# Optimization experiments

Measured on AMD Instinct MI355X. Metric: run time of the kernel, lower is better.

## Reference

```python
import jax, jax.numpy as jnp
import numpy as np

N, GS, M = 128, 4, 64
C_IN, D, L = 128, 512, 8
LIN_D, OUT_DIM = 128, 1


def _gml_layer(G, h, W, b):
    # h: [N,M,C], W: [GS,P,C], b: [GS,P], G: [N,GS,M,M]
    multi = jnp.einsum('nmc,gpc->gnmp', h, W) + b[:, None, None, :]  # [GS,N,M,P]
    xo = jnp.einsum('ngij,gnjp->ngip', G, multi)                      # [N,GS,M,P]
    xo = jax.nn.relu(xo)
    return jnp.max(xo, axis=1)                                        # goodmax over GS


def setup_inputs() -> dict:
    key = jax.random.key(0)
    ks = jax.random.split(key, 12)
    s = 0.05
    return {
        'G': jax.random.uniform(ks[0], (N, GS, M, M), dtype=jnp.float32),
        'x': jax.random.normal(ks[1], (N, M, C_IN), dtype=jnp.float32),
        'W0': jax.random.normal(ks[2], (GS, D, C_IN), dtype=jnp.float32) * s,
        'b0': jax.random.normal(ks[3], (GS, D), dtype=jnp.float32) * s,
        'W': jax.random.normal(ks[4], (L - 1, GS, D, D), dtype=jnp.float32) * s,
        'b': jax.random.normal(ks[5], (L - 1, GS, D), dtype=jnp.float32) * s,
        'lin1_w': jax.random.normal(ks[6], (LIN_D, D), dtype=jnp.float32) * s,
        'lin1_b': jax.random.normal(ks[7], (LIN_D,), dtype=jnp.float32) * s,
        'lin2_w': jax.random.normal(ks[8], (OUT_DIM, LIN_D), dtype=jnp.float32) * s,
        'lin2_b': jax.random.normal(ks[9], (OUT_DIM,), dtype=jnp.float32) * s,
    }


def reference(G, x, W0, b0, W, b, lin1_w, lin1_b, lin2_w, lin2_b):
    # layer 0: C_IN -> D, shapes differ so no residual
    h = _gml_layer(G, x, W0, b0)  # [N,M,D]

    def step(h, wb):
        w, bb = wb
        return _gml_layer(G, h, w, bb) + h, None  # resnet residual (same shape)

    h, _ = jax.lax.scan(step, h, (W, b))  # L-1 layers of D -> D

    x1 = jnp.einsum('nmd,ed->nme', h, lin1_w) + lin1_b
    x2 = jnp.einsum('nme,oe->nmo', jax.nn.relu(x1), lin2_w) + lin2_b
    return x2  # [N, M, OUT_DIM]
```

## Files before the change

kernel.cpp:

```cpp
#include <hip/hip_runtime.h>

typedef float f32x4 __attribute__((ext_vector_type(4)));
typedef short s16x8 __attribute__((ext_vector_type(8)));
typedef short s16x4 __attribute__((ext_vector_type(4)));
typedef int   i32x4 __attribute__((ext_vector_type(4)));

using abfrag = s16x8;

#define DI __device__ __forceinline__

DI unsigned short f2bf(float x) {
  unsigned u = __builtin_bit_cast(unsigned, x);
  u += 0x7fffu + ((u >> 16) & 1u);
  return (unsigned short)(u >> 16);
}
DI float bf2f(unsigned short h) {
  return __builtin_bit_cast(float, ((unsigned)h) << 16);
}

DI f32x4 MFMA(abfrag a, abfrag b, f32x4 c) {
  return __builtin_amdgcn_mfma_f32_16x16x32_bf16(a, b, c, 0, 0, 0);
}

DI void gld16(void* lds_base, const void* gsrc) {
  __builtin_amdgcn_global_load_lds(
      (const __attribute__((address_space(1))) unsigned int*)gsrc,
      (__attribute__((address_space(3))) unsigned int*)lds_base, 16, 0, 0);
}

__global__ void f2bf_multi(const float* __restrict__ s0, int n0,
                           const float* __restrict__ s1, int n1,
                           const float* __restrict__ s2, int n2,
                           const float* __restrict__ s3, int n3,
                           unsigned short* __restrict__ dst) {
  const int total = n0 + n1 + n2 + n3;
  int i = blockIdx.x * blockDim.x + threadIdx.x;
  const int stride = gridDim.x * blockDim.x;
  for (; i < total; i += stride) {
    const float* s; int off;
    if (i < n0) { s = s0; off = i; }
    else if (i < n0 + n1) { s = s1; off = i - n0; }
    else if (i < n0 + n1 + n2) { s = s2; off = i - n0 - n1; }
    else { s = s3; off = i - n0 - n1 - n2; }
    f32x4 v = ((const f32x4*)s)[off];
    s16x4 o;
#pragma unroll
    for (int j = 0; j < 4; ++j) o[j] = (short)f2bf(v[j]);
    ((s16x4*)dst)[i] = o;
  }
}

template <int C, bool RES>
__global__ __launch_bounds__(256, 4) void gml_layer_kernel(
    const unsigned short* __restrict__ hin,
    const unsigned short* __restrict__ Wb,
    const float* __restrict__ bias,
    const unsigned short* __restrict__ Gb,
    unsigned short* __restrict__ hout) {
  constexpr int NT = C / 64;
  __shared__ short lh[64][64];
  __shared__ short lw[4][64][64];

  const int tid  = threadIdx.x;
  const int w    = tid >> 6;
  const int lane = tid & 63;
  const int l15  = lane & 15;
  const int l7   = l15 & 7;
  const int gq   = (lane >> 4) & 3;
  const int n    = blockIdx.x & 127;
  const int pc0  = (blockIdx.x >> 7) * 64;
  const int lrow = lane >> 3;
  const int s8   = lane & 7;
  const int lsoff = ((s8 ^ lrow) << 3);

  const unsigned short* hsrc = hin + (size_t)n * 64 * C;

  f32x4 acc[4][4];
#pragma unroll
  for (int g = 0; g < 4; ++g)
#pragma unroll
    for (int t = 0; t < 4; ++t) acc[g][t] = f32x4{0.f, 0.f, 0.f, 0.f};

  for (int kt = 0; kt < NT; ++kt) {
#pragma unroll
    for (int j = 0; j < 2; ++j)
      gld16(&lh[16 * w + 8 * j][0],
            hsrc + (size_t)(16 * w + 8 * j + lrow) * C + kt * 64 + lsoff);
#pragma unroll
    for (int j = 0; j < 8; ++j)
      gld16(&lw[w][8 * j][0],
            Wb + (size_t)(w * 512 + pc0 + 8 * j + lrow) * C + kt * 64 + lsoff);
    asm volatile("s_waitcnt vmcnt(0)" ::: "memory");
    __syncthreads();

#pragma unroll
    for (int ks = 0; ks < 2; ++ks) {
      const int so = ((4 * ks + gq) ^ l7) << 3;
      abfrag a[4];
#pragma unroll
      for (int t = 0; t < 4; ++t)
        a[t] = *(const abfrag*)&lh[16 * t + l15][so];
#pragma unroll
      for (int g = 0; g < 4; ++g) {
        const abfrag b = *(const abfrag*)&lw[g][16 * w + l15][so];
#pragma unroll
        for (int t = 0; t < 4; ++t) acc[g][t] = MFMA(a[t], b, acc[g][t]);
      }
    }
    __syncthreads();
  }

#pragma unroll
  for (int j = 0; j < 8; ++j)
    gld16(&lw[w][8 * j][0],
          Gb + (size_t)(n * 4 + w) * 4096 + (8 * j + lrow) * 64 + lsoff);
  asm volatile("s_waitcnt vmcnt(0)" ::: "memory");
  __syncthreads();

  float bv[4];
#pragma unroll
  for (int g = 0; g < 4; ++g) bv[g] = bias[g * 512 + pc0 + 16 * w + l15];

  f32x4 xmax[4];
#pragma unroll
  for (int t = 0; t < 4; ++t) xmax[t] = f32x4{0.f, 0.f, 0.f, 0.f};

#pragma unroll
  for (int g = 0; g < 4; ++g) {
    abfrag bb[2];
#pragma unroll
    for (int s = 0; s < 2; ++s) {
      abfrag t8;
#pragma unroll
      for (int r = 0; r < 4; ++r) {
        t8[r]     = (short)f2bf(acc[g][s][r] + bv[g]);
        t8[4 + r] = (short)f2bf(acc[g][s + 2][r] + bv[g]);
      }
      bb[s] = t8;
    }
#pragma unroll
    for (int t = 0; t < 4; ++t) {
      const short* grow = &lw[g][16 * t + l15][0];
      f32x4 xg = f32x4{0.f, 0.f, 0.f, 0.f};
#pragma unroll
      for (int s = 0; s < 2; ++s) {
        const int slot = 2 * s + (gq >> 1);
        const int e1 = ((slot ^ l7) << 3) + ((gq & 1) << 2);
        const int e2 = (((slot + 4) ^ l7) << 3) + ((gq & 1) << 2);
        s16x4 alo = *(const s16x4*)(grow + e1);
        s16x4 ahi = *(const s16x4*)(grow + e2);
        abfrag a;
#pragma unroll
        for (int j = 0; j < 4; ++j) { a[j] = alo[j]; a[4 + j] = ahi[j]; }
        xg = MFMA(a, bb[s], xg);
      }
#pragma unroll
      for (int r = 0; r < 4; ++r)
        xmax[t][r] = fmaxf(xmax[t][r], xg[r]);
    }
  }

  const int d = pc0 + 16 * w + l15;
#pragma unroll
  for (int t = 0; t < 4; ++t)
#pragma unroll
    for (int r = 0; r < 4; ++r) {
      const int m = 16 * t + 4 * gq + r;
      float v = xmax[t][r];
      if constexpr (RES) v += bf2f(hin[(size_t)(n * 64 + m) * C + d]);
      hout[(size_t)(n * 64 + m) * 512 + d] = f2bf(v);
    }
}

__global__ __launch_bounds__(256, 2) void final_kernel(
    const unsigned short* __restrict__ hin,
    const float* __restrict__ w1,
    const float* __restrict__ b1,
    const float* __restrict__ w2,
    const float* __restrict__ b2,
    float* __restrict__ out) {
  constexpr int KT = 64, LW = 72, C = 512, NT = C / KT;
  __shared__ short sh_h[2][64][LW];
  __shared__ short sh_w[2][128][LW];
  __shared__ float red[4][64];
  const int tid = threadIdx.x;
  const int wv  = tid >> 6;
  const int l15 = tid & 15;
  const int gq  = (tid >> 4) & 3;
  const int n   = blockIdx.x;
  const int srow = tid >> 3;
  const int scol = (tid & 7) * 8;
  const unsigned short* hsrc = hin + (size_t)n * 64 * C;

  f32x4 acc[4][2];
#pragma unroll
  for (int t = 0; t < 4; ++t)
#pragma unroll
    for (int u = 0; u < 2; ++u) acc[t][u] = f32x4{0.f, 0.f, 0.f, 0.f};

  i32x4 hr[2], wr[4];
#pragma unroll
  for (int p = 0; p < 2; ++p)
    hr[p] = *(const i32x4*)(hsrc + (srow + p * 32) * C + scol);
#pragma unroll
  for (int p = 0; p < 4; ++p) {
    const float* s = w1 + (srow + p * 32) * C + scol;
    f32x4 v0 = *(const f32x4*)s;
    f32x4 v1 = *(const f32x4*)(s + 4);
    s16x8 o;
#pragma unroll
    for (int j = 0; j < 4; ++j) { o[j] = (short)f2bf(v0[j]); o[4 + j] = (short)f2bf(v1[j]); }
    wr[p] = __builtin_bit_cast(i32x4, o);
  }
#pragma unroll
  for (int p = 0; p < 2; ++p) *(i32x4*)&sh_h[0][srow + p * 32][scol] = hr[p];
#pragma unroll
  for (int p = 0; p < 4; ++p) *(i32x4*)&sh_w[0][srow + p * 32][scol] = wr[p];

  for (int kt = 0; kt < NT; ++kt) {
    const int cur = kt & 1;
    if (kt + 1 < NT) {
#pragma unroll
      for (int p = 0; p < 2; ++p)
        hr[p] = *(const i32x4*)(hsrc + (srow + p * 32) * C + (kt + 1) * KT + scol);
#pragma unroll
      for (int p = 0; p < 4; ++p) {
        const float* s = w1 + (srow + p * 32) * C + (kt + 1) * KT + scol;
        f32x4 v0 = *(const f32x4*)s;
        f32x4 v1 = *(const f32x4*)(s + 4);
        s16x8 o;
#pragma unroll
        for (int j = 0; j < 4; ++j) { o[j] = (short)f2bf(v0[j]); o[4 + j] = (short)f2bf(v1[j]); }
        wr[p] = __builtin_bit_cast(i32x4, o);
      }
    }
    __syncthreads();
#pragma unroll
    for (int ks = 0; ks < 2; ++ks) {
      abfrag a[4], b[2];
#pragma unroll
      for (int t = 0; t < 4; ++t)
        a[t] = *(const abfrag*)&sh_h[cur][16 * t + l15][ks * 32 + gq * 8];
#pragma unroll
      for (int u = 0; u < 2; ++u)
        b[u] = *(const abfrag*)&sh_w[cur][32 * wv + 16 * u + l15][ks * 32 + gq * 8];
#pragma unroll
      for (int t = 0; t < 4; ++t)
#pragma unroll
        for (int u = 0; u < 2; ++u) acc[t][u] = MFMA(a[t], b[u], acc[t][u]);
    }
    if (kt + 1 < NT) {
#pragma unroll
      for (int p = 0; p < 2; ++p) *(i32x4*)&sh_h[1 - cur][srow + p * 32][scol] = hr[p];
#pragma unroll
      for (int p = 0; p < 4; ++p) *(i32x4*)&sh_w[1 - cur][srow + p * 32][scol] = wr[p];
    }
  }

  float b1v[2], w2v[2];
#pragma unroll
  for (int u = 0; u < 2; ++u) {
    b1v[u] = b1[32 * wv + 16 * u + l15];
    w2v[u] = w2[32 * wv + 16 * u + l15];
  }
  float part[4][4];
#pragma unroll
  for (int t = 0; t < 4; ++t)
#pragma unroll
    for (int r = 0; r < 4; ++r) {
      float s0 = 0.f;
#pragma unroll
      for (int u = 0; u < 2; ++u)
        s0 += fmaxf(acc[t][u][r] + b1v[u], 0.f) * w2v[u];
      part[t][r] = s0;
    }
#pragma unroll
  for (int t = 0; t < 4; ++t)
#pragma unroll
    for (int r = 0; r < 4; ++r)
#pragma unroll
      for (int msk = 1; msk < 16; msk <<= 1)
        part[t][r] += __shfl_xor(part[t][r], msk);
  if (l15 == 0) {
#pragma unroll
    for (int t = 0; t < 4; ++t)
#pragma unroll
      for (int r = 0; r < 4; ++r) red[wv][16 * t + 4 * gq + r] = part[t][r];
  }
  __syncthreads();
  if (tid < 64)
    out[(size_t)n * 64 + tid] =
        red[0][tid] + red[1][tid] + red[2][tid] + red[3][tid] + b2[0];
}

extern "C" void kernel_launch(void* const* d_in, const int* in_sizes, int n_in,
                              void* d_out, int out_size, void* d_ws, size_t ws_size,
                              hipStream_t stream) {
  const float* G   = (const float*)d_in[0];
  const float* x   = (const float*)d_in[1];
  const float* W0  = (const float*)d_in[2];
  const float* b0  = (const float*)d_in[3];
  const float* W   = (const float*)d_in[4];
  const float* b   = (const float*)d_in[5];
  const float* l1w = (const float*)d_in[6];
  const float* l1b = (const float*)d_in[7];
  const float* l2w = (const float*)d_in[8];
  const float* l2b = (const float*)d_in[9];
  float* out = (float*)d_out;

  char* p = (char*)d_ws;
  unsigned short* W0b = (unsigned short*)p; p += (size_t)4 * 512 * 128 * 2;
  unsigned short* Wb  = (unsigned short*)p; p += (size_t)7 * 4 * 512 * 512 * 2;
  unsigned short* Gb  = (unsigned short*)p; p += (size_t)128 * 4 * 64 * 64 * 2;
  unsigned short* xb  = (unsigned short*)p; p += (size_t)128 * 64 * 128 * 2;
  unsigned short* hA  = (unsigned short*)p; p += (size_t)128 * 64 * 512 * 2;
  unsigned short* hB  = (unsigned short*)p; p += (size_t)128 * 64 * 512 * 2;

  const int n0 = 4 * 512 * 128 / 4;
  const int n1 = 7 * 4 * 512 * 512 / 4;
  const int n2 = 128 * 4 * 64 * 64 / 4;
  const int n3 = 128 * 64 * 128 / 4;
  f2bf_multi<<<4096, 256, 0, stream>>>(W0, n0, W, n1, G, n2, x, n3, W0b);

  gml_layer_kernel<128, false><<<1024, 256, 0, stream>>>(xb, W0b, b0, Gb, hA);
  const unsigned short* src = hA;
  unsigned short* dst = hB;
  for (int i = 0; i < 7; ++i) {
    gml_layer_kernel<512, true><<<1024, 256, 0, stream>>>(
        src, Wb + (size_t)i * 4 * 512 * 512, b + (size_t)i * 4 * 512, Gb, dst);
    const unsigned short* t = src; src = dst; dst = (unsigned short*)t;
  }
  final_kernel<<<128, 256, 0, stream>>>(src, l1w, l1b, l2w, l2b, out);
}
```

Baseline: 211.3 us.

## Process two graphs per block to share weight tiles; read G directly from global

Result: slower. 353.8 us (+67.4%).

```diff
diff --git a/kernel.cpp b/kernel.cpp
--- a/kernel.cpp
+++ b/kernel.cpp
@@ -51,14 +51,14 @@
 }
 
 template <int C, bool RES>
-__global__ __launch_bounds__(256, 4) void gml_layer_kernel(
+__global__ __launch_bounds__(512, 4) void gml_layer_kernel(
     const unsigned short* __restrict__ hin,
     const unsigned short* __restrict__ Wb,
     const float* __restrict__ bias,
     const unsigned short* __restrict__ Gb,
     unsigned short* __restrict__ hout) {
   constexpr int NT = C / 64;
-  __shared__ short lh[64][64];
+  __shared__ short lh[2][64][64];
   __shared__ short lw[4][64][64];
 
   const int tid  = threadIdx.x;
@@ -67,13 +67,22 @@
   const int l15  = lane & 15;
   const int l7   = l15 & 7;
   const int gq   = (lane >> 4) & 3;
-  const int n    = blockIdx.x & 127;
-  const int pc0  = (blockIdx.x >> 7) * 64;
+  const int nl   = w >> 2;
+  const int cv   = w & 3;
+  const int nn   = blockIdx.x & 63;
+  const int pc0  = (blockIdx.x >> 6) * 64;
+  const int n    = 2 * nn + nl;
   const int lrow = lane >> 3;
   const int s8   = lane & 7;
   const int lsoff = ((s8 ^ lrow) << 3);
 
   const unsigned short* hsrc = hin + (size_t)n * 64 * C;
+  const int shn = w >> 2, shr = 16 * (w & 3);
+  const int swg = w & 3, swr = 32 * (w >> 2);
+  const unsigned short* hstage =
+      hin + ((size_t)(2 * nn + shn) * 64 + shr + lrow) * C + lsoff;
+  const unsigned short* wstage =
+      Wb + (size_t)(swg * 512 + pc0 + swr + lrow) * C + lsoff;
 
   f32x4 acc[4][4];
 #pragma unroll
@@ -84,12 +93,10 @@
   for (int kt = 0; kt < NT; ++kt) {
 #pragma unroll
     for (int j = 0; j < 2; ++j)
-      gld16(&lh[16 * w + 8 * j][0],
-            hsrc + (size_t)(16 * w + 8 * j + lrow) * C + kt * 64 + lsoff);
-#pragma unroll
-    for (int j = 0; j < 8; ++j)
-      gld16(&lw[w][8 * j][0],
-            Wb + (size_t)(w * 512 + pc0 + 8 * j + lrow) * C + kt * 64 + lsoff);
+      gld16(&lh[shn][shr + 8 * j][0], hstage + (size_t)(8 * j) * C + kt * 64);
+#pragma unroll
+    for (int j = 0; j < 4; ++j)
+      gld16(&lw[swg][swr + 8 * j][0], wstage + (size_t)(8 * j) * C + kt * 64);
     asm volatile("s_waitcnt vmcnt(0)" ::: "memory");
     __syncthreads();
 
@@ -99,10 +106,10 @@
       abfrag a[4];
 #pragma unroll
       for (int t = 0; t < 4; ++t)
-        a[t] = *(const abfrag*)&lh[16 * t + l15][so];
+        a[t] = *(const abfrag*)&lh[nl][16 * t + l15][so];
 #pragma unroll
       for (int g = 0; g < 4; ++g) {
-        const abfrag b = *(const abfrag*)&lw[g][16 * w + l15][so];
+        const abfrag b = *(const abfrag*)&lw[g][16 * cv + l15][so];
 #pragma unroll
         for (int t = 0; t < 4; ++t) acc[g][t] = MFMA(a[t], b, acc[g][t]);
       }
@@ -110,21 +117,15 @@
     __syncthreads();
   }
 
-#pragma unroll
-  for (int j = 0; j < 8; ++j)
-    gld16(&lw[w][8 * j][0],
-          Gb + (size_t)(n * 4 + w) * 4096 + (8 * j + lrow) * 64 + lsoff);
-  asm volatile("s_waitcnt vmcnt(0)" ::: "memory");
-  __syncthreads();
-
   float bv[4];
 #pragma unroll
-  for (int g = 0; g < 4; ++g) bv[g] = bias[g * 512 + pc0 + 16 * w + l15];
+  for (int g = 0; g < 4; ++g) bv[g] = bias[g * 512 + pc0 + 16 * cv + l15];
 
   f32x4 xmax[4];
 #pragma unroll
   for (int t = 0; t < 4; ++t) xmax[t] = f32x4{0.f, 0.f, 0.f, 0.f};
 
+  const unsigned short* gbase = Gb + (size_t)n * 4 * 4096;
 #pragma unroll
   for (int g = 0; g < 4; ++g) {
     abfrag bb[2];
@@ -138,17 +139,15 @@
       }
       bb[s] = t8;
     }
+    const unsigned short* gg = gbase + g * 4096;
 #pragma unroll
     for (int t = 0; t < 4; ++t) {
-      const short* grow = &lw[g][16 * t + l15][0];
       f32x4 xg = f32x4{0.f, 0.f, 0.f, 0.f};
 #pragma unroll
       for (int s = 0; s < 2; ++s) {
-        const int slot = 2 * s + (gq >> 1);
-        const int e1 = ((slot ^ l7) << 3) + ((gq & 1) << 2);
-        const int e2 = (((slot + 4) ^ l7) << 3) + ((gq & 1) << 2);
-        s16x4 alo = *(const s16x4*)(grow + e1);
-        s16x4 ahi = *(const s16x4*)(grow + e2);
+        const unsigned short* gp = gg + (16 * t + l15) * 64 + 16 * s + 4 * gq;
+        s16x4 alo = *(const s16x4*)gp;
+        s16x4 ahi = *(const s16x4*)(gp + 32);
         abfrag a;
 #pragma unroll
         for (int j = 0; j < 4; ++j) { a[j] = alo[j]; a[4 + j] = ahi[j]; }
@@ -160,7 +159,7 @@
     }
   }
 
-  const int d = pc0 + 16 * w + l15;
+  const int d = pc0 + 16 * cv + l15;
 #pragma unroll
   for (int t = 0; t < 4; ++t)
 #pragma unroll
@@ -322,11 +321,11 @@
   const int n3 = 128 * 64 * 128 / 4;
   f2bf_multi<<<4096, 256, 0, stream>>>(W0, n0, W, n1, G, n2, x, n3, W0b);
 
-  gml_layer_kernel<128, false><<<1024, 256, 0, stream>>>(xb, W0b, b0, Gb, hA);
+  gml_layer_kernel<128, false><<<512, 512, 0, stream>>>(xb, W0b, b0, Gb, hA);
   const unsigned short* src = hA;
   unsigned short* dst = hB;
   for (int i = 0; i < 7; ++i) {
-    gml_layer_kernel<512, true><<<1024, 256, 0, stream>>>(
+    gml_layer_kernel<512, true><<<512, 512, 0, stream>>>(
         src, Wb + (size_t)i * 4 * 512 * 512, b + (size_t)i * 4 * 512, Gb, dst);
     const unsigned short* t = src; src = dst; dst = (unsigned short*)t;
   }
```
